# Kernel optimization log

Hardware: AMD Instinct MI355X
Metric: run time of the kernel (lower is better)

The kernel has to match this reference:

```python
import jax, jax.numpy as jnp
import numpy as np
import math

B, L, DM, H, ALPHA = 8, 2048, 512, 8, 3
DH = DM // H
SK = min(ALPHA * math.ceil(math.log(L)), L)    # sample_k = U_part = 24
NTOP = min(ALPHA * math.ceil(math.log(L)), L)  # n_top u = 24


def _ln(x, w, b, eps=1e-8):
    # TF-style layernorm (eps inside sqrt), matching custom LayerNorm
    u = x.mean(-1, keepdims=True)
    s = ((x - u) ** 2).mean(-1, keepdims=True)
    return w * (x - u) / jnp.sqrt(s + eps) + b


def setup_inputs() -> dict:
    key = jax.random.key(0)
    ks = jax.random.split(key, 12)
    p = lambda k, shape: jax.random.normal(k, shape, dtype=jnp.float32) * 0.02
    return {
        'queries': jax.random.normal(ks[0], (B, L, DM), dtype=jnp.float32),
        'keys': jax.random.normal(ks[1], (B, L, DM), dtype=jnp.float32),
        'values': jax.random.normal(ks[2], (B, L, DM), dtype=jnp.float32),
        'padding_mask': jnp.ones((B, L), dtype=jnp.float32),
        'Wq': p(ks[3], (DM, DM)), 'bq': jnp.zeros((DM,), jnp.float32),
        'Wk': p(ks[4], (DM, DM)), 'bk': jnp.zeros((DM,), jnp.float32),
        'Wv': p(ks[5], (DM, DM)), 'bv': jnp.zeros((DM,), jnp.float32),
        'Wf': p(ks[6], (DM, DM)), 'bf': jnp.zeros((DM,), jnp.float32),
        'qln_w': jnp.ones((DM,), jnp.float32), 'qln_b': jnp.zeros((DM,), jnp.float32),
        'fln_w': jnp.ones((DM,), jnp.float32), 'fln_b': jnp.zeros((DM,), jnp.float32),
        'index_sample': jax.random.randint(ks[7], (L, SK), 0, L, dtype=jnp.int32),
    }


def reference(queries, keys, values, padding_mask, Wq, bq, Wk, bk, Wv, bv, Wf, bf,
              qln_w, qln_b, fln_w, fln_b, index_sample):
    Bq, Lq, Dm = queries.shape
    Lk = keys.shape[1]
    Dh = Dm // H
    # projections + head split -> (B, H, L, Dh)
    q = (_ln(queries, qln_w, qln_b) @ Wq + bq).reshape(Bq, Lq, H, Dh).transpose(0, 2, 1, 3)
    k = (keys @ Wk + bk).reshape(Bq, Lk, H, Dh).transpose(0, 2, 1, 3)
    v = (values @ Wv + bv).reshape(Bq, Lk, H, Dh).transpose(0, 2, 1, 3)
    # _prob_QK: random K sampling + sparsity measure + top-n_top query selection
    K_sample = k[:, :, index_sample, :]                        # (B,H,Lq,SK,Dh) irregular gather
    QKs = jnp.einsum('bhid,bhijd->bhij', q, K_sample)          # (B,H,Lq,SK)
    M = QKs.max(-1) - QKs.sum(-1) / Lk
    _, m_top = jax.lax.top_k(M, NTOP)                          # (B,H,u)
    q_red = jnp.take_along_axis(q, m_top[..., None], axis=2)   # (B,H,u,Dh)
    # NOTE: source scales by 1/sqrt(full hidden dim D), not head size
    scores = jnp.einsum('bhud,bhkd->bhuk', q_red, k) * (1.0 / math.sqrt(Dm))
    # ProbMask: causal (key <= selected query pos) AND padding at selected queries
    causal = jnp.arange(Lk)[None, None, None, :] <= m_top[..., None]   # (B,H,u,Lk)
    pad_ind = padding_mask[jnp.arange(Bq)[:, None, None], m_top]       # (B,H,u)
    mask = causal & (pad_ind[..., None] != 0)
    scores = jnp.where(mask, scores, -100000.0)
    # initial values = causal cumulative mean of V (with_mask branch)
    v_avg = jnp.cumsum(v, axis=2) / (jnp.cumsum(padding_mask, -1)[:, None, :, None] + 1e-12)
    attn = jax.nn.softmax(scores, axis=-1)
    upd = jnp.einsum('bhuk,bhkd->bhud', attn, v)               # sparse attention output
    bi = jnp.arange(Bq)[:, None, None]
    hi = jnp.arange(H)[None, :, None]
    out = v_avg.at[bi, hi, m_top].set(upd)                     # scatter selected rows back
    out = out.transpose(0, 2, 1, 3).reshape(Bq, Lq, Dm)
    out = out @ Wf + bf
    return _ln(out, fln_w, fln_b)
```

## Files before the change

### kernel.cpp

```cpp
#include <hip/hip_runtime.h>
#include <math.h>

#define L 2048
#define DM 512
#define B_ 8
#define H_ 8
#define DH 64
#define SK 24
#define NTOP 24
#define CHUNK 128
#define NCH (L / CHUNK)
#define VC 32
#define VR 64
#define ABUF 4096

typedef __attribute__((ext_vector_type(8))) short short8;
typedef __attribute__((ext_vector_type(8))) __bf16 bf16x8;
typedef __attribute__((ext_vector_type(4))) float f32x4;

__device__ inline unsigned short f2bf(float x) {
    unsigned u = __float_as_uint(x);
    unsigned r = (u + 0x7FFFu + ((u >> 16) & 1u)) >> 16;
    return (unsigned short)r;
}
__device__ inline float bf2f(unsigned short h) {
    return __uint_as_float(((unsigned)h) << 16);
}

__device__ inline f32x4 MFMA_BF16(short8 a, short8 b, f32x4 c) {
    return __builtin_amdgcn_mfma_f32_16x16x32_bf16(
        __builtin_bit_cast(bf16x8, a), __builtin_bit_cast(bf16x8, b), c, 0, 0, 0);
}

template<bool WANTL>
__device__ inline void cvt8(const float4& x, const float4& y, short8& h, short8& l) {
    float v0 = x.x, v1 = x.y, v2 = x.z, v3 = x.w;
    float v4 = y.x, v5 = y.y, v6 = y.z, v7 = y.w;
    unsigned short h0 = f2bf(v0), h1 = f2bf(v1), h2 = f2bf(v2), h3 = f2bf(v3);
    unsigned short h4 = f2bf(v4), h5 = f2bf(v5), h6 = f2bf(v6), h7 = f2bf(v7);
    h[0] = (short)h0; h[1] = (short)h1; h[2] = (short)h2; h[3] = (short)h3;
    h[4] = (short)h4; h[5] = (short)h5; h[6] = (short)h6; h[7] = (short)h7;
    if (WANTL) {
        l[0] = (short)f2bf(v0 - bf2f(h0)); l[1] = (short)f2bf(v1 - bf2f(h1));
        l[2] = (short)f2bf(v2 - bf2f(h2)); l[3] = (short)f2bf(v3 - bf2f(h3));
        l[4] = (short)f2bf(v4 - bf2f(h4)); l[5] = (short)f2bf(v5 - bf2f(h5));
        l[6] = (short)f2bf(v6 - bf2f(h6)); l[7] = (short)f2bf(v7 - bf2f(h7));
    }
}

__device__ inline int lds_addr(int row, int kblk) {
    return row * 32 + ((kblk ^ ((row >> 1) & 3)) << 3);
}

__device__ inline float waveReduceSum(float v) {
    for (int o = 32; o > 0; o >>= 1) v += __shfl_down(v, o, 64);
    return v;
}
__device__ inline float waveReduceMax(float v) {
    for (int o = 32; o > 0; o >>= 1) v = fmaxf(v, __shfl_down(v, o, 64));
    return v;
}

__global__ __launch_bounds__(256)
void ln_kernel(const float* __restrict__ x, const float* __restrict__ w,
               const float* __restrict__ bvec, float* __restrict__ out) {
    int row = blockIdx.x;
    const float* xr = x + (size_t)row * DM;
    float* orow = out + (size_t)row * DM;
    int tid = threadIdx.x;
    float2 v = *(const float2*)(xr + tid * 2);
    float s = v.x + v.y;
    float sq = v.x * v.x + v.y * v.y;
    __shared__ float red[8];
    float ws = waveReduceSum(s);
    float wq = waveReduceSum(sq);
    int wid = tid >> 6, lane = tid & 63;
    if (lane == 0) { red[wid] = ws; red[4 + wid] = wq; }
    __syncthreads();
    float tot = red[0] + red[1] + red[2] + red[3];
    float totq = red[4] + red[5] + red[6] + red[7];
    float mean = tot * (1.0f / DM);
    float var = totq * (1.0f / DM) - mean * mean;
    float inv = rsqrtf(var + 1e-8f);
    float w0 = w[tid * 2], w1 = w[tid * 2 + 1];
    float b0 = bvec[tid * 2], b1 = bvec[tid * 2 + 1];
    float2 o;
    o.x = w0 * (v.x - mean) * inv + b0;
    o.y = w1 * (v.y - mean) * inv + b1;
    *(float2*)(orow + tid * 2) = o;
}

__global__ __launch_bounds__(256)
void ln_split_kernel(const float* __restrict__ x, const float* __restrict__ w,
                     const float* __restrict__ bvec,
                     unsigned short* __restrict__ oh, unsigned short* __restrict__ ol) {
    int row = blockIdx.x;
    const float* xr = x + (size_t)row * DM;
    int tid = threadIdx.x;
    float2 v = *(const float2*)(xr + tid * 2);
    float s = v.x + v.y;
    float sq = v.x * v.x + v.y * v.y;
    __shared__ float red[8];
    float ws = waveReduceSum(s);
    float wq = waveReduceSum(sq);
    int wid = tid >> 6, lane = tid & 63;
    if (lane == 0) { red[wid] = ws; red[4 + wid] = wq; }
    __syncthreads();
    float tot = red[0] + red[1] + red[2] + red[3];
    float totq = red[4] + red[5] + red[6] + red[7];
    float mean = tot * (1.0f / DM);
    float var = totq * (1.0f / DM) - mean * mean;
    float inv = rsqrtf(var + 1e-8f);
    float w0 = w[tid * 2], w1 = w[tid * 2 + 1];
    float b0 = bvec[tid * 2], b1 = bvec[tid * 2 + 1];
    float o0 = w0 * (v.x - mean) * inv + b0;
    float o1 = w1 * (v.y - mean) * inv + b1;
    ushort2 hh, ll;
    hh.x = f2bf(o0); ll.x = f2bf(o0 - bf2f(hh.x));
    hh.y = f2bf(o1); ll.y = f2bf(o1 - bf2f(hh.y));
    *(ushort2*)(oh + (size_t)row * DM + tid * 2) = hh;
    *(ushort2*)(ol + (size_t)row * DM + tid * 2) = ll;
}

__global__ __launch_bounds__(256)
void wsplit_kernel(const float* __restrict__ W, unsigned short* __restrict__ th,
                   unsigned short* __restrict__ tl) {
    __shared__ float ts[32][33];
    int k0 = blockIdx.y * 32, n0 = blockIdx.x * 32;
    int t = threadIdx.x;
    int r = t >> 3, c = (t & 7) * 4;
    float4 v = *(const float4*)(W + (size_t)(k0 + r) * 512 + n0 + c);
    ts[r][c] = v.x; ts[r][c + 1] = v.y; ts[r][c + 2] = v.z; ts[r][c + 3] = v.w;
    __syncthreads();
    float a0 = ts[c + 0][r], a1 = ts[c + 1][r], a2 = ts[c + 2][r], a3 = ts[c + 3][r];
    ushort4 h, l;
    h.x = f2bf(a0); l.x = f2bf(a0 - bf2f(h.x));
    h.y = f2bf(a1); l.y = f2bf(a1 - bf2f(h.y));
    h.z = f2bf(a2); l.z = f2bf(a2 - bf2f(h.z));
    h.w = f2bf(a3); l.w = f2bf(a3 - bf2f(h.w));
    *(ushort4*)(th + (size_t)(n0 + r) * 512 + k0 + c) = h;
    *(ushort4*)(tl + (size_t)(n0 + r) * 512 + k0 + c) = l;
}

template<int TERMS, int OMODE, int ACVT>
__device__ __forceinline__
void gemm_body(unsigned short* smem,
               const unsigned short* __restrict__ Ah, const unsigned short* __restrict__ Al,
               const float* __restrict__ Af,
               const unsigned short* __restrict__ Bh, const unsigned short* __restrict__ Bl,
               const float* __restrict__ bias, float* __restrict__ C,
               unsigned short* __restrict__ Ch, int orig) {
    unsigned short* sAh = smem;
    unsigned short* sAl = smem + 2 * ABUF;
    unsigned short* sBh = smem + (TERMS == 3 ? 4 : 2) * ABUF;
    unsigned short* sBl = sBh + 2 * ABUF;

    int j = (orig & 7) * 64 + (orig >> 3);
    int n0 = (j & 3) * 128, m0 = (j >> 2) * 128;

    int tid = threadIdx.x;
    int lane = tid & 63, wv = tid >> 6;
    int wr = wv >> 1, wc = wv & 1;
    int lrow = lane & 15, g = lane >> 4;

    int f0 = tid, f1 = tid + 256;
    int row0 = f0 >> 2, k0b = f0 & 3;
    int row1 = f1 >> 2, k1b = f1 & 3;
    int sa0 = lds_addr(row0, k0b), sa1 = lds_addr(row1, k1b);
    int c0 = k0b * 8, c1 = k1b * 8;

    f32x4 acc[4][4];
#pragma unroll
    for (int mf = 0; mf < 4; mf++)
#pragma unroll
        for (int nf = 0; nf < 4; nf++) acc[mf][nf] = (f32x4){0.f, 0.f, 0.f, 0.f};

    short8 rAh0, rAh1, rAl0, rAl1, rBh0, rBh1, rBl0, rBl1;
    float4 fA00, fA01, fA10, fA11;

    auto LOAD = [&](int kt) {
        int k0 = kt * 32;
        if (ACVT) {
            fA00 = *(const float4*)(Af + (size_t)(m0 + row0) * 512 + k0 + c0);
            fA01 = *(const float4*)(Af + (size_t)(m0 + row0) * 512 + k0 + c0 + 4);
            fA10 = *(const float4*)(Af + (size_t)(m0 + row1) * 512 + k0 + c1);
            fA11 = *(const float4*)(Af + (size_t)(m0 + row1) * 512 + k0 + c1 + 4);
        } else {
            rAh0 = *(const short8*)(Ah + (size_t)(m0 + row0) * 512 + k0 + c0);
            rAh1 = *(const short8*)(Ah + (size_t)(m0 + row1) * 512 + k0 + c1);
            if (TERMS == 3) {
                rAl0 = *(const short8*)(Al + (size_t)(m0 + row0) * 512 + k0 + c0);
                rAl1 = *(const short8*)(Al + (size_t)(m0 + row1) * 512 + k0 + c1);
            }
        }
        rBh0 = *(const short8*)(Bh + (size_t)(n0 + row0) * 512 + k0 + c0);
        rBh1 = *(const short8*)(Bh + (size_t)(n0 + row1) * 512 + k0 + c1);
        if (TERMS >= 2) {
            rBl0 = *(const short8*)(Bl + (size_t)(n0 + row0) * 512 + k0 + c0);
            rBl1 = *(const short8*)(Bl + (size_t)(n0 + row1) * 512 + k0 + c1);
        }
    };
    auto STORE = [&](int buf) {
        int o = buf * ABUF;
        if (ACVT) {
            cvt8<TERMS == 3>(fA00, fA01, rAh0, rAl0);
            cvt8<TERMS == 3>(fA10, fA11, rAh1, rAl1);
        }
        *(short8*)&sAh[o + sa0] = rAh0;
        *(short8*)&sAh[o + sa1] = rAh1;
        if (TERMS == 3) {
            *(short8*)&sAl[o + sa0] = rAl0;
            *(short8*)&sAl[o + sa1] = rAl1;
        }
        *(short8*)&sBh[o + sa0] = rBh0;
        *(short8*)&sBh[o + sa1] = rBh1;
        if (TERMS >= 2) {
            *(short8*)&sBl[o + sa0] = rBl0;
            *(short8*)&sBl[o + sa1] = rBl1;
        }
    };

    int ra = wr * 64 + lrow;
    int rb = wc * 64 + lrow;
    int abase = ra * 32 + ((g ^ ((ra >> 1) & 3)) << 3);
    int bbase = rb * 32 + ((g ^ ((rb >> 1) & 3)) << 3);

    LOAD(0);
    STORE(0);
    for (int kt = 0; kt < 16; kt++) {
        int co = (kt & 1) * ABUF;
        __syncthreads();
        if (kt < 15) LOAD(kt + 1);
        short8 ah[4], al[4], bh[4], bl[4];
#pragma unroll
        for (int mf = 0; mf < 4; mf++) {
            ah[mf] = *(const short8*)&sAh[co + abase + mf * 512];
            if (TERMS == 3) al[mf] = *(const short8*)&sAl[co + abase + mf * 512];
        }
#pragma unroll
        for (int nf = 0; nf < 4; nf++) {
            bh[nf] = *(const short8*)&sBh[co + bbase + nf * 512];
            if (TERMS >= 2) bl[nf] = *(const short8*)&sBl[co + bbase + nf * 512];
        }
#pragma unroll
        for (int mf = 0; mf < 4; mf++)
#pragma unroll
            for (int nf = 0; nf < 4; nf++) {
                acc[mf][nf] = MFMA_BF16(ah[mf], bh[nf], acc[mf][nf]);
                if (TERMS >= 2) acc[mf][nf] = MFMA_BF16(ah[mf], bl[nf], acc[mf][nf]);
                if (TERMS == 3) acc[mf][nf] = MFMA_BF16(al[mf], bh[nf], acc[mf][nf]);
            }
        if (kt < 15) STORE((kt & 1) ^ 1);
    }

    int crow0 = m0 + wr * 64 + (lane >> 4) * 4;
    int ccol0 = n0 + wc * 64 + lrow;
    float bb[4];
#pragma unroll
    for (int nf = 0; nf < 4; nf++) bb[nf] = bias[ccol0 + nf * 16];
#pragma unroll
    for (int mf = 0; mf < 4; mf++)
#pragma unroll
        for (int nf = 0; nf < 4; nf++)
#pragma unroll
            for (int r = 0; r < 4; r++) {
                float val = acc[mf][nf][r] + bb[nf];
                size_t idx = (size_t)(crow0 + mf * 16 + r) * 512 + ccol0 + nf * 16;
                if (OMODE != 2) C[idx] = val;
                if (OMODE != 0) Ch[idx] = f2bf(val);
            }
}

__global__ __launch_bounds__(256, 2)
void qkv_gemm(const unsigned short* __restrict__ lnq_h, const unsigned short* __restrict__ lnq_l,
              const float* __restrict__ keys, const float* __restrict__ values,
              const unsigned short* __restrict__ wq_h, const unsigned short* __restrict__ wq_l,
              const unsigned short* __restrict__ wk_h, const unsigned short* __restrict__ wk_l,
              const unsigned short* __restrict__ wv_h, const unsigned short* __restrict__ wv_l,
              const float* __restrict__ bq, const float* __restrict__ bk, const float* __restrict__ bv,
              float* __restrict__ qb, float* __restrict__ kb,
              unsigned short* __restrict__ kb_h, unsigned short* __restrict__ vb_h) {
    __shared__ __align__(16) unsigned short smem[8 * ABUF];
    int orig = blockIdx.x + 4 * blockIdx.y;
    if (blockIdx.z == 0)
        gemm_body<3, 0, 0>(smem, lnq_h, lnq_l, nullptr, wq_h, wq_l, bq, qb, nullptr, orig);
    else if (blockIdx.z == 1)
        gemm_body<3, 1, 1>(smem, nullptr, nullptr, keys, wk_h, wk_l, bk, kb, kb_h, orig);
    else
        gemm_body<1, 2, 1>(smem, nullptr, nullptr, values, wv_h, wv_l, bv, nullptr, vb_h, orig);
}

template<int TERMS, int OMODE, int ACVT>
__global__ __launch_bounds__(256, 2)
void gemm_mfma(const unsigned short* __restrict__ Ah, const unsigned short* __restrict__ Al,
               const float* __restrict__ Af,
               const unsigned short* __restrict__ Bh, const unsigned short* __restrict__ Bl,
               const float* __restrict__ bias, float* __restrict__ C,
               unsigned short* __restrict__ Ch) {
    __shared__ __align__(16) unsigned short smem[4 * ABUF];
    int orig = blockIdx.x + 4 * blockIdx.y;
    gemm_body<TERMS, OMODE, ACVT>(smem, Ah, Al, Af, Bh, Bl, bias, C, Ch, orig);
}

__global__ __launch_bounds__(256)
void sample_m_kernel(const float* __restrict__ q, const float* __restrict__ k,
                     const int* __restrict__ idx, float* __restrict__ M) {
    int bid = blockIdx.x;
    int b = bid & 7;
    int ig = bid >> 3;
    int wv = threadIdx.x >> 6, lane = threadIdx.x & 63;
    int i = ig * 4 + wv;
    const float* qrow = q + ((size_t)b * L + i) * DM + lane * 8;
    float4 q0 = *(const float4*)qrow;
    float4 q1 = *(const float4*)(qrow + 4);
    int myidx = 0;
    if (lane < SK) myidx = idx[i * SK + lane];
    float sj[SK];
#pragma unroll
    for (int j = 0; j < SK; j++) {
        int row = __shfl(myidx, j, 64);
        const float* kp = k + ((size_t)b * L + row) * DM + lane * 8;
        float4 k0 = *(const float4*)kp;
        float4 k1 = *(const float4*)(kp + 4);
        sj[j] = q0.x * k0.x + q0.y * k0.y + q0.z * k0.z + q0.w * k0.w
              + q1.x * k1.x + q1.y * k1.y + q1.z * k1.z + q1.w * k1.w;
    }
    float mx = -1e30f, sm = 0.f;
#pragma unroll
    for (int j = 0; j < SK; j++) {
        float s = sj[j];
        s += __shfl_xor(s, 1, 64);
        s += __shfl_xor(s, 2, 64);
        s += __shfl_xor(s, 4, 64);
        mx = fmaxf(mx, s);
        sm += s;
    }
    if ((lane & 7) == 0) {
        int h = lane >> 3;
        M[((size_t)b * H_ + h) * L + i] = mx - sm * (1.0f / L);
    }
}

__global__ __launch_bounds__(64)
void topk_kernel(const float* __restrict__ M, const float* __restrict__ qb,
                 const float* __restrict__ pad, int* __restrict__ mtop,
                 unsigned short* __restrict__ qsel, int* __restrict__ lim_arr) {
    int bh = blockIdx.x;
    int b = bh >> 3, h = bh & 7;
    int lane = threadIdx.x;
    const float* Mr = M + (size_t)bh * L;
    __shared__ int sel_s[NTOP];
    float m[32];
#pragma unroll
    for (int r = 0; r < 32; r++) m[r] = Mr[r * 64 + lane];
    for (int it = 0; it < NTOP; it++) {
        float bv = -1e30f; int br = 0;
#pragma unroll
        for (int r = 0; r < 32; r++) {
            bool better = m[r] > bv;
            br = better ? r : br;
            bv = better ? m[r] : bv;
        }
        int bt = (br << 6) | lane;
#pragma unroll
        for (int o = 1; o < 64; o <<= 1) {
            float ov = __shfl_xor(bv, o, 64);
            int ot = __shfl_xor(bt, o, 64);
            bool take = (ov > bv) || (ov == bv && ot < bt);
            bv = take ? ov : bv;
            bt = take ? ot : bt;
        }
        if (lane == 0) { mtop[bh * NTOP + it] = bt; sel_s[it] = bt; }
        int rwin = bt >> 6;
        bool mine = (bt & 63) == lane;
#pragma unroll
        for (int r = 0; r < 32; r++)
            if (mine && (r == rwin)) m[r] = -1e30f;
    }
    __syncthreads();
    for (int u = 0; u < NTOP; u++) {
        int iq = sel_s[u];
        bool ok = pad[(size_t)b * L + iq] != 0.f;
        float sc = ok ? 0.044194173824159216f : 0.f;
        float qv = qb[((size_t)b * L + iq) * DM + h * DH + lane];
        qsel[((size_t)bh * 32 + u) * 64 + lane] = f2bf(qv * sc);
        if (lane == 0) lim_arr[bh * 32 + u] = ok ? iq : (L - 1);
    }
    for (int u = NTOP; u < 32; u++) {
        qsel[((size_t)bh * 32 + u) * 64 + lane] = 0;
        if (lane == 0) lim_arr[bh * 32 + u] = -1;
    }
}

__global__ __launch_bounds__(256)
void padscan_kernel(const float* __restrict__ pad, float* __restrict__ denom) {
    int b = blockIdx.x;
    __shared__ float tot[256];
    int tid = threadIdx.x;
    const float* p = pad + (size_t)b * L;
    float loc[8];
    float s = 0.f;
#pragma unroll
    for (int u = 0; u < 8; u++) { s += p[tid * 8 + u]; loc[u] = s; }
    tot[tid] = s;
    __syncthreads();
    for (int off = 1; off < 256; off <<= 1) {
        float add = (tid >= off) ? tot[tid - off] : 0.f;
        __syncthreads();
        tot[tid] += add;
        __syncthreads();
    }
    float excl = tot[tid] - s;
#pragma unroll
    for (int u = 0; u < 8; u++) denom[(size_t)b * L + tid * 8 + u] = excl + loc[u];
}

__global__ __launch_bounds__(256)
void vsum_kernel(const unsigned short* __restrict__ vh, float* __restrict__ csum) {
    int c = blockIdx.x, b = blockIdx.y;
    int d2 = threadIdx.x;
    size_t base = ((size_t)b * L + c * VR) * DM + d2 * 2;
    float a0 = 0.f, a1 = 0.f;
    for (int t = 0; t < VR; t++) {
        unsigned v = *(const unsigned*)(vh + base + (size_t)t * DM);
        a0 += bf2f((unsigned short)(v & 0xffff));
        a1 += bf2f((unsigned short)(v >> 16));
    }
    float2 st = {a0, a1};
    *(float2*)(csum + ((size_t)b * VC + c) * DM + d2 * 2) = st;
}

__global__ __launch_bounds__(256)
void vavg_kernel(const unsigned short* __restrict__ vh, const float* __restrict__ csum,
                 const float* __restrict__ denom, unsigned short* __restrict__ out_h) {
    int c = blockIdx.x, b = blockIdx.y;
    int d2 = threadIdx.x;
    float a0 = 0.f, a1 = 0.f;
    for (int cc = 0; cc < c; cc++) {
        float2 t = *(const float2*)(csum + ((size_t)b * VC + cc) * DM + d2 * 2);
        a0 += t.x; a1 += t.y;
    }
    size_t base = ((size_t)b * L + c * VR) * DM + d2 * 2;
    for (int t = 0; t < VR; t++) {
        unsigned v = *(const unsigned*)(vh + base + (size_t)t * DM);
        a0 += bf2f((unsigned short)(v & 0xffff));
        a1 += bf2f((unsigned short)(v >> 16));
        float dn = denom[(size_t)b * L + c * VR + t] + 1e-12f;
        unsigned o = (unsigned)f2bf(a0 / dn) | ((unsigned)f2bf(a1 / dn) << 16);
        *(unsigned*)(out_h + base + (size_t)t * DM) = o;
    }
}

__global__ __launch_bounds__(256)
void attn_chunk_mfma(const unsigned short* __restrict__ kbh,
                     const unsigned short* __restrict__ vbh,
                     const unsigned short* __restrict__ qsel,
                     const int* __restrict__ lim_arr,
                     float* __restrict__ part_m, float* __restrict__ part_s,
                     float* __restrict__ part_acc) {
    int c = blockIdx.x, bh = blockIdx.y;
    int b = bh >> 3, h = bh & 7;
    int j0 = c * CHUNK;
    __shared__ __align__(16) unsigned short KV[128 * 64];
    __shared__ __align__(16) unsigned short Ps[32 * 128];
    __shared__ __align__(16) unsigned short Qs[32 * 64];
    __shared__ float redm[4][32];
    __shared__ float reds[4][32];
    __shared__ int lims[32];

    int tid = threadIdx.x;
    int wv = tid >> 6, lane = tid & 63;
    int l15 = lane & 15, g = lane >> 4;

    const unsigned short* kpanel = kbh + ((size_t)b * L + j0) * DM + h * DH;
    short8 kreg[4];
#pragma unroll
    for (int l = 0; l < 4; l++) {
        int f = tid + l * 256;
        int jr = f >> 3, blk = f & 7;
        kreg[l] = *(const short8*)(kpanel + (size_t)jr * DM + blk * 8);
    }
    {
        int u = tid >> 3, blk = tid & 7;
        short8 qreg = *(const short8*)(qsel + ((size_t)bh * 32 + u) * 64 + blk * 8);
        *(short8*)&Qs[u * 64 + (((blk ^ (u & 7))) << 3)] = qreg;
    }
#pragma unroll
    for (int l = 0; l < 4; l++) {
        int f = tid + l * 256;
        int jr = f >> 3, blk = f & 7;
        *(short8*)&KV[jr * 64 + ((blk ^ (jr & 7)) << 3)] = kreg[l];
    }
    if (tid < 32) lims[tid] = lim_arr[bh * 32 + tid];
    __syncthreads();

    f32x4 sf[2][2];
#pragma unroll
    for (int mf = 0; mf < 2; mf++)
#pragma unroll
        for (int nf = 0; nf < 2; nf++) sf[mf][nf] = (f32x4){0.f, 0.f, 0.f, 0.f};
#pragma unroll
    for (int ks = 0; ks < 2; ks++) {
        short8 aq[2], bk[2];
#pragma unroll
        for (int mf = 0; mf < 2; mf++) {
            int u = mf * 16 + l15;
            int blk = (ks * 4 + g) ^ (u & 7);
            aq[mf] = *(const short8*)&Qs[u * 64 + (blk << 3)];
        }
#pragma unroll
        for (int nf = 0; nf < 2; nf++) {
            int jr = wv * 32 + nf * 16 + l15;
            int blk = (ks * 4 + g) ^ (jr & 7);
            bk[nf] = *(const short8*)&KV[jr * 64 + (blk << 3)];
        }
#pragma unroll
        for (int mf = 0; mf < 2; mf++)
#pragma unroll
            for (int nf = 0; nf < 2; nf++)
                sf[mf][nf] = MFMA_BF16(aq[mf], bk[nf], sf[mf][nf]);
    }

    const unsigned short* vpanel = vbh + ((size_t)b * L + j0) * DM + h * DH;
    short8 vreg[4];
#pragma unroll
    for (int l = 0; l < 4; l++) {
        int f = tid + l * 256;
        int jr = f >> 3, blk = f & 7;
        vreg[l] = *(const short8*)(vpanel + (size_t)jr * DM + blk * 8);
    }

    float sv[2][2][4];
    float mx[2][4];
#pragma unroll
    for (int mf = 0; mf < 2; mf++)
#pragma unroll
        for (int r = 0; r < 4; r++) {
            int u = mf * 16 + g * 4 + r;
            int limv = lims[u];
            float m = -1e30f;
#pragma unroll
            for (int nf = 0; nf < 2; nf++) {
                int jg = j0 + wv * 32 + nf * 16 + l15;
                float s = (jg <= limv) ? sf[mf][nf][r] : -1e30f;
                sv[mf][nf][r] = s;
                m = fmaxf(m, s);
            }
            m = fmaxf(m, __shfl_xor(m, 1, 64));
            m = fmaxf(m, __shfl_xor(m, 2, 64));
            m = fmaxf(m, __shfl_xor(m, 4, 64));
            m = fmaxf(m, __shfl_xor(m, 8, 64));
            mx[mf][r] = m;
        }
    if (l15 == 0) {
#pragma unroll
        for (int mf = 0; mf < 2; mf++)
#pragma unroll
            for (int r = 0; r < 4; r++)
                redm[wv][mf * 16 + g * 4 + r] = mx[mf][r];
    }
    __syncthreads();

    float lmax[2][4], smv[2][4];
#pragma unroll
    for (int mf = 0; mf < 2; mf++)
#pragma unroll
        for (int r = 0; r < 4; r++) {
            int u = mf * 16 + g * 4 + r;
            float m = fmaxf(fmaxf(redm[0][u], redm[1][u]),
                            fmaxf(redm[2][u], redm[3][u]));
            lmax[mf][r] = m;
            bool any = m > -1e29f;
            float sm = 0.f;
#pragma unroll
            for (int nf = 0; nf < 2; nf++) {
                float e = any ? __expf(sv[mf][nf][r] - m) : 0.f;
                sm += e;
                int jr = wv * 32 + nf * 16 + l15;
                Ps[u * 128 + (((jr >> 3) ^ (u & 7)) << 3) + (jr & 7)] = f2bf(e);
            }
            sm += __shfl_xor(sm, 1, 64);
            sm += __shfl_xor(sm, 2, 64);
            sm += __shfl_xor(sm, 4, 64);
            sm += __shfl_xor(sm, 8, 64);
            smv[mf][r] = sm;
        }
    if (l15 == 0) {
#pragma unroll
        for (int mf = 0; mf < 2; mf++)
#pragma unroll
            for (int r = 0; r < 4; r++)
                reds[wv][mf * 16 + g * 4 + r] = smv[mf][r];
    }
#pragma unroll
    for (int l = 0; l < 4; l++) {
        int f = tid + l * 256;
        int jr = f >> 3, blk = f & 7;
        short8 w = vreg[l];
        if ((jr >> 3) & 1) w = __builtin_shufflevector(w, w, 4, 5, 6, 7, 0, 1, 2, 3);
        *(short8*)&KV[jr * 64 + ((blk ^ (jr & 7)) << 3)] = w;
    }
    __syncthreads();

    if (wv == 0 && l15 == 0) {
#pragma unroll
        for (int mf = 0; mf < 2; mf++)
#pragma unroll
            for (int r = 0; r < 4; r++) {
                int u = mf * 16 + g * 4 + r;
                if (u < NTOP) {
                    float ss = reds[0][u] + reds[1][u] + reds[2][u] + reds[3][u];
                    part_m[(bh * NTOP + u) * NCH + c] = lmax[mf][r];
                    part_s[(bh * NTOP + u) * NCH + c] = ss;
                }
            }
    }

    f32x4 of[2];
    of[0] = (f32x4){0.f, 0.f, 0.f, 0.f};
    of[1] = (f32x4){0.f, 0.f, 0.f, 0.f};
    int d = wv * 16 + l15;
#pragma unroll
    for (int ks = 0; ks < 4; ks++) {
        unsigned short va[8];
#pragma unroll
        for (int i = 0; i < 8; i++) {
            int jr = ks * 32 + g * 8 + i;
            int addr = jr * 64 + (((d >> 3) ^ (jr & 7)) << 3)
                     + ((d & 7) ^ (((jr >> 3) & 1) << 2));
            va[i] = KV[addr];
        }
        short8 av;
#pragma unroll
        for (int i = 0; i < 8; i++) av[i] = (short)va[i];
        short8 bp[2];
#pragma unroll
        for (int nf = 0; nf < 2; nf++) {
            int u = nf * 16 + l15;
            int blk = (ks * 4 + g) ^ (u & 7);
            bp[nf] = *(const short8*)&Ps[u * 128 + (blk << 3)];
        }
#pragma unroll
        for (int nf = 0; nf < 2; nf++)
            of[nf] = MFMA_BF16(av, bp[nf], of[nf]);
    }
#pragma unroll
    for (int nf = 0; nf < 2; nf++) {
        int u = nf * 16 + l15;
        if (u < NTOP) {
#pragma unroll
            for (int r = 0; r < 4; r++)
                part_acc[((size_t)(bh * NTOP + u) * NCH + c) * 64 + wv * 16 + g * 4 + r] =
                    of[nf][r];
        }
    }
}

__global__ __launch_bounds__(256)
void attn_merge_kernel(const float* __restrict__ part_m, const float* __restrict__ part_s,
                       const float* __restrict__ part_acc, const int* __restrict__ mtop,
                       unsigned short* __restrict__ pre_h) {
    int ug = blockIdx.x;
    int bh = blockIdx.y;
    int b = bh >> 3, h = bh & 7;
    int tid = threadIdx.x;
    int u = ug * 4 + (tid >> 6);
    int d = tid & 63;
    int base = (bh * NTOP + u) * NCH;
    float m = -1e30f;
#pragma unroll
    for (int c = 0; c < NCH; c++) m = fmaxf(m, part_m[base + c]);
    float s = 0.f, o = 0.f;
#pragma unroll
    for (int c = 0; c < NCH; c++) {
        float w = __expf(part_m[base + c] - m);
        s += part_s[base + c] * w;
        o = fmaf(part_acc[(size_t)(base + c) * 64 + d], w, o);
    }
    o /= s;
    int iq = mtop[bh * NTOP + u];
    pre_h[((size_t)b * L + iq) * DM + h * DH + d] = f2bf(o);
}

extern "C" void kernel_launch(void* const* d_in, const int* in_sizes, int n_in,
                              void* d_out, int out_size, void* d_ws, size_t ws_size,
                              hipStream_t stream) {
    const float* queries = (const float*)d_in[0];
    const float* keys    = (const float*)d_in[1];
    const float* values  = (const float*)d_in[2];
    const float* pad     = (const float*)d_in[3];
    const float* Wq = (const float*)d_in[4];  const float* bq = (const float*)d_in[5];
    const float* Wk = (const float*)d_in[6];  const float* bk = (const float*)d_in[7];
    const float* Wv = (const float*)d_in[8];  const float* bv = (const float*)d_in[9];
    const float* Wf = (const float*)d_in[10]; const float* bfv = (const float*)d_in[11];
    const float* qlnw = (const float*)d_in[12]; const float* qlnb = (const float*)d_in[13];
    const float* flnw = (const float*)d_in[14]; const float* flnb = (const float*)d_in[15];
    const int* idx = (const int*)d_in[16];

    float* ws = (float*)d_ws;
    const size_t NE = (size_t)B_ * L * DM;
    float* qb    = ws;
    float* kb    = ws + NE;
    unsigned short* vb_h = (unsigned short*)(ws + 2 * NE);
    unsigned short* kb_h = vb_h + NE;
    unsigned short* qsel = (unsigned short*)(ws + 3 * NE);
    int* lim_arr = (int*)(qsel + 64 * 32 * 64);
    float* Mbuf  = ws + 4 * NE;
    float* denom = Mbuf + (size_t)B_ * H_ * L;
    float* csum  = denom + (size_t)B_ * L;
    int*   mtop  = (int*)(csum + (size_t)B_ * VC * DM);
    unsigned short* bfr = (unsigned short*)(mtop + 2048);
    unsigned short* pre_h = bfr;
    unsigned short* wts   = bfr + NE;
    unsigned short* wq_h = wts;              unsigned short* wq_l = wts + 262144;
    unsigned short* wk_h = wts + 2 * 262144; unsigned short* wk_l = wts + 3 * 262144;
    unsigned short* wv_h = wts + 4 * 262144; unsigned short* wv_l = wts + 5 * 262144;
    unsigned short* wf_h = wts + 6 * 262144; unsigned short* wf_l = wts + 7 * 262144;

    float* tmp = (float*)d_out;
    unsigned short* lnq_h = (unsigned short*)d_out;
    unsigned short* lnq_l = lnq_h + NE;
    float* part_m   = tmp;
    float* part_s   = part_m + 64 * NTOP * NCH;
    float* part_acc = part_s + 64 * NTOP * NCH;

    padscan_kernel<<<B_, 256, 0, stream>>>(pad, denom);
    ln_split_kernel<<<B_ * L, 256, 0, stream>>>(queries, qlnw, qlnb, lnq_h, lnq_l);
    dim3 gw(16, 16);
    wsplit_kernel<<<gw, 256, 0, stream>>>(Wq, wq_h, wq_l);
    wsplit_kernel<<<gw, 256, 0, stream>>>(Wk, wk_h, wk_l);
    wsplit_kernel<<<gw, 256, 0, stream>>>(Wv, wv_h, wv_l);
    wsplit_kernel<<<gw, 256, 0, stream>>>(Wf, wf_h, wf_l);

    dim3 gq(4, 128, 3);
    qkv_gemm<<<gq, 256, 0, stream>>>(lnq_h, lnq_l, keys, values,
                                     wq_h, wq_l, wk_h, wk_l, wv_h, wv_l,
                                     bq, bk, bv, qb, kb, kb_h, vb_h);

    sample_m_kernel<<<B_ * L / 4, 256, 0, stream>>>(qb, kb, idx, Mbuf);
    topk_kernel<<<B_ * H_, 64, 0, stream>>>(Mbuf, qb, pad, mtop, qsel, lim_arr);
    dim3 gv(VC, B_);
    vsum_kernel<<<gv, 256, 0, stream>>>(vb_h, csum);
    vavg_kernel<<<gv, 256, 0, stream>>>(vb_h, csum, denom, pre_h);
    dim3 gc(NCH, 64);
    attn_chunk_mfma<<<gc, 256, 0, stream>>>(kb_h, vb_h, qsel, lim_arr,
                                            part_m, part_s, part_acc);
    dim3 gmg(6, 64);
    attn_merge_kernel<<<gmg, 256, 0, stream>>>(part_m, part_s, part_acc, mtop, pre_h);
    dim3 gg(4, 128);
    gemm_mfma<1, 0, 0><<<gg, 256, 0, stream>>>(pre_h, nullptr, nullptr, wf_h, wf_l, bfv, (float*)d_out, nullptr);
    ln_kernel<<<B_ * L, 256, 0, stream>>>((float*)d_out, flnw, flnb, (float*)d_out);
}
```

Measured before the change: 260.6 us.

## Replace double-buffered LDS tiles with single buffer and two barriers per k-step

The GEMM body moves from two LDS buffers per operand to a single buffer. Each k-iteration now stores the prefetched registers, synchronises, issues the next global load, computes, then synchronises again. This halves shared memory (64KB to 32KB in qkv_gemm), which may allow more resident blocks per CU. In exchange it adds a second barrier per iteration and drops the overlap between the LDS store of the next tile and the current MFMA work.

```diff
diff --git a/kernel.cpp b/kernel.cpp
--- a/kernel.cpp
+++ b/kernel.cpp
@@ -151,9 +151,9 @@
                const float* __restrict__ bias, float* __restrict__ C,
                unsigned short* __restrict__ Ch, int orig) {
     unsigned short* sAh = smem;
-    unsigned short* sAl = smem + 2 * ABUF;
-    unsigned short* sBh = smem + (TERMS == 3 ? 4 : 2) * ABUF;
-    unsigned short* sBl = sBh + 2 * ABUF;
+    unsigned short* sAl = smem + ABUF;
+    unsigned short* sBh = smem + (TERMS == 3 ? 2 : 1) * ABUF;
+    unsigned short* sBl = sBh + ABUF;
 
     int j = (orig & 7) * 64 + (orig >> 3);
     int n0 = (j & 3) * 128, m0 = (j >> 2) * 128;
@@ -200,23 +200,22 @@
             rBl1 = *(const short8*)(Bl + (size_t)(n0 + row1) * 512 + k0 + c1);
         }
     };
-    auto STORE = [&](int buf) {
-        int o = buf * ABUF;
+    auto STORE = [&]() {
         if (ACVT) {
             cvt8<TERMS == 3>(fA00, fA01, rAh0, rAl0);
             cvt8<TERMS == 3>(fA10, fA11, rAh1, rAl1);
         }
-        *(short8*)&sAh[o + sa0] = rAh0;
-        *(short8*)&sAh[o + sa1] = rAh1;
+        *(short8*)&sAh[sa0] = rAh0;
+        *(short8*)&sAh[sa1] = rAh1;
         if (TERMS == 3) {
-            *(short8*)&sAl[o + sa0] = rAl0;
-            *(short8*)&sAl[o + sa1] = rAl1;
-        }
-        *(short8*)&sBh[o + sa0] = rBh0;
-        *(short8*)&sBh[o + sa1] = rBh1;
+            *(short8*)&sAl[sa0] = rAl0;
+            *(short8*)&sAl[sa1] = rAl1;
+        }
+        *(short8*)&sBh[sa0] = rBh0;
+        *(short8*)&sBh[sa1] = rBh1;
         if (TERMS >= 2) {
-            *(short8*)&sBl[o + sa0] = rBl0;
-            *(short8*)&sBl[o + sa1] = rBl1;
+            *(short8*)&sBl[sa0] = rBl0;
+            *(short8*)&sBl[sa1] = rBl1;
         }
     };
 
@@ -226,21 +225,20 @@
     int bbase = rb * 32 + ((g ^ ((rb >> 1) & 3)) << 3);
 
     LOAD(0);
-    STORE(0);
     for (int kt = 0; kt < 16; kt++) {
-        int co = (kt & 1) * ABUF;
+        STORE();
         __syncthreads();
         if (kt < 15) LOAD(kt + 1);
         short8 ah[4], al[4], bh[4], bl[4];
 #pragma unroll
         for (int mf = 0; mf < 4; mf++) {
-            ah[mf] = *(const short8*)&sAh[co + abase + mf * 512];
-            if (TERMS == 3) al[mf] = *(const short8*)&sAl[co + abase + mf * 512];
+            ah[mf] = *(const short8*)&sAh[abase + mf * 512];
+            if (TERMS == 3) al[mf] = *(const short8*)&sAl[abase + mf * 512];
         }
 #pragma unroll
         for (int nf = 0; nf < 4; nf++) {
-            bh[nf] = *(const short8*)&sBh[co + bbase + nf * 512];
-            if (TERMS >= 2) bl[nf] = *(const short8*)&sBl[co + bbase + nf * 512];
+            bh[nf] = *(const short8*)&sBh[bbase + nf * 512];
+            if (TERMS >= 2) bl[nf] = *(const short8*)&sBl[bbase + nf * 512];
         }
 #pragma unroll
         for (int mf = 0; mf < 4; mf++)
@@ -250,7 +248,7 @@
                 if (TERMS >= 2) acc[mf][nf] = MFMA_BF16(ah[mf], bl[nf], acc[mf][nf]);
                 if (TERMS == 3) acc[mf][nf] = MFMA_BF16(al[mf], bh[nf], acc[mf][nf]);
             }
-        if (kt < 15) STORE((kt & 1) ^ 1);
+        __syncthreads();
     }
 
     int crow0 = m0 + wr * 64 + (lane >> 4) * 4;
@@ -280,7 +278,7 @@
               const float* __restrict__ bq, const float* __restrict__ bk, const float* __restrict__ bv,
               float* __restrict__ qb, float* __restrict__ kb,
               unsigned short* __restrict__ kb_h, unsigned short* __restrict__ vb_h) {
-    __shared__ __align__(16) unsigned short smem[8 * ABUF];
+    __shared__ __align__(16) unsigned short smem[4 * ABUF];
     int orig = blockIdx.x + 4 * blockIdx.y;
     if (blockIdx.z == 0)
         gemm_body<3, 0, 0>(smem, lnq_h, lnq_l, nullptr, wq_h, wq_l, bq, qb, nullptr, orig);
@@ -297,7 +295,7 @@
                const unsigned short* __restrict__ Bh, const unsigned short* __restrict__ Bl,
                const float* __restrict__ bias, float* __restrict__ C,
                unsigned short* __restrict__ Ch) {
-    __shared__ __align__(16) unsigned short smem[4 * ABUF];
+    __shared__ __align__(16) unsigned short smem[(TERMS == 3 ? 4 : (TERMS == 2 ? 3 : 2)) * ABUF];
     int orig = blockIdx.x + 4 * blockIdx.y;
     gemm_body<TERMS, OMODE, ACVT>(smem, Ah, Al, Af, Bh, Bl, bias, C, Ch, orig);
 }
```

Result: no change. 256.2 us (-1.7%).
